# Performance work log

Hardware: AMD Instinct MI355X
Metric: run time of the kernel (lower is better)

Reference implementation:

```python
import jax, jax.numpy as jnp
import numpy as np

B, O, I = 128, 1024, 1024
EPS = 1e-07

def setup_inputs() -> dict:
    key = jax.random.key(0)
    ks = jax.random.split(key, 7)
    data = jax.random.normal(ks[0], (B, I), dtype=jnp.float32)
    # parameters, matching torch init: 2*rand-1, rand+0.1, 2*rand-1, ones+0.1, rand, rand
    input_x = 2.0 * jax.random.uniform(ks[1], (1, O, I), dtype=jnp.float32) - 1.0
    input_y = jax.random.uniform(ks[2], (1, O, I), dtype=jnp.float32) + 0.1
    output_x = 2.0 * jax.random.uniform(ks[3], (1, O, I), dtype=jnp.float32) - 1.0
    output_y = jnp.ones((1, O, I), dtype=jnp.float32) + 0.1
    linkage_add = jax.random.uniform(ks[4], (1, O, I), dtype=jnp.float32)
    linkage_mul = jax.random.uniform(ks[5], (1, O, I), dtype=jnp.float32)
    return {"data": data, "input_x": input_x, "input_y": input_y,
            "output_x": output_x, "output_y": output_y,
            "linkage_add": linkage_add, "linkage_mul": linkage_mul}

def reference(data, input_x, input_y, output_x, output_y, linkage_add, linkage_mul):
    shape = data.shape
    d = data.reshape(-1, 1, I)                      # (B,1,I)
    inp = input_x / input_y                          # (1,O,I)
    out = output_x / output_y                        # (1,O,I)
    tests = (inp + linkage_add) * (1.0 + linkage_mul)
    error = (tests - out) * jax.nn.sigmoid(d)        # (B,O,I)
    w = jax.nn.softmax(1.0 / jnp.sqrt(error * error + EPS), axis=1)
    expect = d * w                                   # (B,O,I)
    return jnp.sum(expect, axis=2).reshape(shape)
```

## Files before the change

### kernel.cpp

```cpp
#include <hip/hip_runtime.h>

#define B_ 128
#define O_ 1024
#define I_ 1024
#define NCHUNK 64
#define CI (I_ / NCHUNK)
#define WPB 4
#define TT_BYTES ((size_t)O_ * I_ * sizeof(float))

#define LOG2E_F  1.4426950408889634f
#define LN2_F    0.6931471805599453f
#define LN2SQ_F  0.4804530139182014f
#define EPSC_F   (1e-7f * LN2SQ_F)

typedef float v2f __attribute__((ext_vector_type(2)));

__device__ __forceinline__ float fast_rsq(float x)  { return __builtin_amdgcn_rsqf(x); }
__device__ __forceinline__ float fast_exp2(float x) { return __builtin_amdgcn_exp2f(x); }
__device__ __forceinline__ float fast_rcp(float x)  { return __builtin_amdgcn_rcpf(x); }

__device__ __forceinline__ float rfl(float x) {
    return __builtin_bit_cast(float,
        __builtin_amdgcn_readfirstlane(__builtin_bit_cast(int, x)));
}

template <int CTRL>
__device__ __forceinline__ float dpp_add(float v) {
    int x = __builtin_amdgcn_update_dpp(0, __builtin_bit_cast(int, v),
                                        CTRL, 0xf, 0xf, true);
    return v + __builtin_bit_cast(float, x);
}
__device__ __forceinline__ float wave_sum_uniform(float v) {
    v = dpp_add<0xB1>(v);
    v = dpp_add<0x4E>(v);
    v = dpp_add<0x141>(v);
    v = dpp_add<0x140>(v);
    v = dpp_add<0x142>(v);
    v = dpp_add<0x143>(v);
    return __builtin_bit_cast(float,
        __builtin_amdgcn_readlane(__builtin_bit_cast(int, v), 63));
}

__global__ __launch_bounds__(256) void build_T2_kernel(
    const float* __restrict__ ix, const float* __restrict__ iy,
    const float* __restrict__ ox, const float* __restrict__ oy,
    const float* __restrict__ la, const float* __restrict__ lm,
    float* __restrict__ Tt2, unsigned* __restrict__ minbits,
    float* __restrict__ out_zero)
{
    __shared__ float tile[32][33];
    __shared__ unsigned mloc[32];
    const int i0 = blockIdx.x * 32;
    const int o0 = blockIdx.y * 32;
    const int tx = threadIdx.x;
    const int ty = threadIdx.y;
    const int t  = ty * 32 + tx;

    if (t < 32) mloc[t] = 0xFFFFFFFFu;

    const int bid = blockIdx.y * gridDim.x + blockIdx.x;
    if (t < 128) out_zero[bid * 128 + t] = 0.0f;

#pragma unroll
    for (int r = 0; r < 32; r += 8) {
        const int o = o0 + ty + r;
        const int i = i0 + tx;
        const int idx = o * I_ + i;
        const float tt = fmaf(ix[idx] * fast_rcp(iy[idx]) + la[idx],
                              1.0f + lm[idx],
                              -(ox[idx] * fast_rcp(oy[idx])));
        tile[ty + r][tx] = tt * tt;
    }
    __syncthreads();
#pragma unroll
    for (int r = 0; r < 32; r += 8) {
        const int i = i0 + ty + r;
        const int o = o0 + tx;
        Tt2[i * O_ + o] = tile[tx][ty + r];
    }
    const int il = t & 31;
    const int g  = t >> 5;
    float mn = fminf(fminf(tile[4 * g + 0][il], tile[4 * g + 1][il]),
                     fminf(tile[4 * g + 2][il], tile[4 * g + 3][il]));
    atomicMin(&mloc[il], __builtin_bit_cast(unsigned, mn));
    __syncthreads();
    if (t < 32) atomicMin(&minbits[i0 + t], mloc[t]);
}

__global__ __launch_bounds__(256) void aeg_main_kernel(
    const float* __restrict__ data,
    const float* __restrict__ Tt2,
    const float* __restrict__ minr2,
    float* __restrict__ out)
{
    __shared__ float red[WPB][O_];

    const int w    = threadIdx.x >> 6;
    const int lane = threadIdx.x & 63;
    const int chunk = blockIdx.x * WPB + w;
    const int b     = blockIdx.y;

    const float4* rowbase = (const float4*)(Tt2 + (size_t)chunk * CI * O_);

    const float4* dv4 = (const float4*)(data + b * I_ + chunk * CI);
    const float4* mr4 = (const float4*)(minr2 + chunk * CI);
    float sdv[CI], ss2[CI], sm2[CI];
#pragma unroll
    for (int k = 0; k < 4; ++k) {
        const float4 a = dv4[k];
        const float4 m = mr4[k];
        const float av[4] = {a.x, a.y, a.z, a.w};
        const float mv[4] = {m.x, m.y, m.z, m.w};
#pragma unroll
        for (int j = 0; j < 4; ++j) {
            const float dv  = av[j];
            const float sig = fast_rcp(1.0f + fast_exp2(-dv * LOG2E_F));
            const float sc  = sig * LN2_F;
            const float s2  = sc * sc;
            const float m2  = fast_rsq(fmaf(mv[j], s2, EPSC_F));
            sdv[4 * k + j] = rfl(dv);
            ss2[4 * k + j] = rfl(s2);
            sm2[4 * k + j] = rfl(m2);
        }
    }

    v2f acc2[8];
#pragma unroll
    for (int j = 0; j < 8; ++j) acc2[j] = (v2f)0.0f;

    float4 rr[2][4];
#pragma unroll
    for (int k = 0; k < 4; ++k) rr[0][k] = rowbase[lane + 64 * k];

#pragma unroll
    for (int ii = 0; ii < CI; ++ii) {
        if (ii + 1 < CI) {
            const float4* nrow = rowbase + (size_t)(ii + 1) * (O_ / 4);
#pragma unroll
            for (int k = 0; k < 4; ++k) rr[(ii + 1) & 1][k] = nrow[lane + 64 * k];
        }
        float4* r = rr[ii & 1];
        const v2f s2v = {ss2[ii], ss2[ii]};
        const v2f m2v = {sm2[ii], sm2[ii]};
        const v2f epv = {EPSC_F, EPSC_F};

        v2f zv0 = (v2f)0.0f, zv1 = (v2f)0.0f;
#pragma unroll
        for (int k = 0; k < 4; ++k) {
            const v2f a = {r[k].x, r[k].y};
            const v2f c = {r[k].z, r[k].w};
            const v2f q0 = a * s2v + epv;
            const v2f q1 = c * s2v + epv;
            v2f t0, t1;
            t0.x = fast_rsq(q0.x); t0.y = fast_rsq(q0.y);
            t1.x = fast_rsq(q1.x); t1.y = fast_rsq(q1.y);
            t0 -= m2v;
            t1 -= m2v;
            r[k].x = fast_exp2(t0.x); r[k].y = fast_exp2(t0.y);
            r[k].z = fast_exp2(t1.x); r[k].w = fast_exp2(t1.y);
            zv0 += (v2f){r[k].x, r[k].y};
            zv1 += (v2f){r[k].z, r[k].w};
        }
        const v2f zv = zv0 + zv1;
        const float zt = wave_sum_uniform(zv.x + zv.y);
        const float scale = sdv[ii] * fast_rcp(zt);
        const v2f sc2 = {scale, scale};
#pragma unroll
        for (int k = 0; k < 4; ++k) {
            acc2[2 * k]     = (v2f){r[k].x, r[k].y} * sc2 + acc2[2 * k];
            acc2[2 * k + 1] = (v2f){r[k].z, r[k].w} * sc2 + acc2[2 * k + 1];
        }
    }

#pragma unroll
    for (int k = 0; k < 4; ++k) {
        float4 v;
        v.x = acc2[2 * k].x;     v.y = acc2[2 * k].y;
        v.z = acc2[2 * k + 1].x; v.w = acc2[2 * k + 1].y;
        ((float4*)&red[w][256 * k])[lane] = v;
    }
    __syncthreads();

    const int t = threadIdx.x;
    float4 v = ((const float4*)red[0])[t];
#pragma unroll
    for (int ww = 1; ww < WPB; ++ww) {
        const float4 u = ((const float4*)red[ww])[t];
        v.x += u.x; v.y += u.y; v.z += u.z; v.w += u.w;
    }
    float* ob = out + b * O_ + 4 * t;
    atomicAdd(&ob[0], v.x);
    atomicAdd(&ob[1], v.y);
    atomicAdd(&ob[2], v.z);
    atomicAdd(&ob[3], v.w);
}

extern "C" void kernel_launch(void* const* d_in, const int* in_sizes, int n_in,
                              void* d_out, int out_size, void* d_ws, size_t ws_size,
                              hipStream_t stream)
{
    const float* data = (const float*)d_in[0];
    const float* ix   = (const float*)d_in[1];
    const float* iy   = (const float*)d_in[2];
    const float* ox   = (const float*)d_in[3];
    const float* oy   = (const float*)d_in[4];
    const float* la   = (const float*)d_in[5];
    const float* lm   = (const float*)d_in[6];
    float* out  = (float*)d_out;
    float* Tt2  = (float*)d_ws;
    unsigned* minbits = (unsigned*)((char*)d_ws + TT_BYTES);

    (void)hipMemsetAsync(minbits, 0xFF, I_ * sizeof(unsigned), stream);

    build_T2_kernel<<<dim3(I_ / 32, O_ / 32), dim3(32, 8), 0, stream>>>(
        ix, iy, ox, oy, la, lm, Tt2, minbits, out);

    aeg_main_kernel<<<dim3(NCHUNK / WPB, B_), 256, 0, stream>>>(
        data, Tt2, (const float*)minbits, out);
}
```

Before: 122.0 us.

## Process two batch rows per wave to reuse each loaded T2 row

```diff
diff --git a/kernel.cpp b/kernel.cpp
--- a/kernel.cpp
+++ b/kernel.cpp
@@ -3,9 +3,10 @@
 #define B_ 128
 #define O_ 1024
 #define I_ 1024
-#define NCHUNK 64
+#define NCHUNK 128
 #define CI (I_ / NCHUNK)
 #define WPB 4
+#define BPW 2
 #define TT_BYTES ((size_t)O_ * I_ * sizeof(float))
 
 #define LOG2E_F  1.4426950408889634f
@@ -98,101 +99,164 @@
     const int w    = threadIdx.x >> 6;
     const int lane = threadIdx.x & 63;
     const int chunk = blockIdx.x * WPB + w;
-    const int b     = blockIdx.y;
+    const int b0    = blockIdx.y * BPW;
+    const int b1    = b0 + 1;
 
     const float4* rowbase = (const float4*)(Tt2 + (size_t)chunk * CI * O_);
 
-    const float4* dv4 = (const float4*)(data + b * I_ + chunk * CI);
+    const float4* d04 = (const float4*)(data + b0 * I_ + chunk * CI);
+    const float4* d14 = (const float4*)(data + b1 * I_ + chunk * CI);
     const float4* mr4 = (const float4*)(minr2 + chunk * CI);
-    float sdv[CI], ss2[CI], sm2[CI];
-#pragma unroll
-    for (int k = 0; k < 4; ++k) {
-        const float4 a = dv4[k];
-        const float4 m = mr4[k];
-        const float av[4] = {a.x, a.y, a.z, a.w};
-        const float mv[4] = {m.x, m.y, m.z, m.w};
+    float sdv0[CI], ss20[CI], sm20[CI];
+    float sdv1[CI], ss21[CI], sm21[CI];
+#pragma unroll
+    for (int k = 0; k < 2; ++k) {
+        const float4 a0 = d04[k];
+        const float4 a1 = d14[k];
+        const float4 m  = mr4[k];
+        const float a0v[4] = {a0.x, a0.y, a0.z, a0.w};
+        const float a1v[4] = {a1.x, a1.y, a1.z, a1.w};
+        const float mv[4]  = {m.x,  m.y,  m.z,  m.w};
 #pragma unroll
         for (int j = 0; j < 4; ++j) {
-            const float dv  = av[j];
-            const float sig = fast_rcp(1.0f + fast_exp2(-dv * LOG2E_F));
-            const float sc  = sig * LN2_F;
-            const float s2  = sc * sc;
-            const float m2  = fast_rsq(fmaf(mv[j], s2, EPSC_F));
-            sdv[4 * k + j] = rfl(dv);
-            ss2[4 * k + j] = rfl(s2);
-            sm2[4 * k + j] = rfl(m2);
-        }
-    }
-
-    v2f acc2[8];
-#pragma unroll
-    for (int j = 0; j < 8; ++j) acc2[j] = (v2f)0.0f;
-
-    float4 rr[2][4];
-#pragma unroll
-    for (int k = 0; k < 4; ++k) rr[0][k] = rowbase[lane + 64 * k];
+            const int idx = 4 * k + j;
+            {
+                const float dv  = a0v[j];
+                const float sig = fast_rcp(1.0f + fast_exp2(-dv * LOG2E_F));
+                const float sc  = sig * LN2_F;
+                const float s2  = sc * sc;
+                sdv0[idx] = rfl(dv);
+                ss20[idx] = rfl(s2);
+                sm20[idx] = rfl(fast_rsq(fmaf(mv[j], s2, EPSC_F)));
+            }
+            {
+                const float dv  = a1v[j];
+                const float sig = fast_rcp(1.0f + fast_exp2(-dv * LOG2E_F));
+                const float sc  = sig * LN2_F;
+                const float s2  = sc * sc;
+                sdv1[idx] = rfl(dv);
+                ss21[idx] = rfl(s2);
+                sm21[idx] = rfl(fast_rsq(fmaf(mv[j], s2, EPSC_F)));
+            }
+        }
+    }
+
+    v2f acc0[8], acc1[8];
+#pragma unroll
+    for (int j = 0; j < 8; ++j) { acc0[j] = (v2f)0.0f; acc1[j] = (v2f)0.0f; }
 
 #pragma unroll
     for (int ii = 0; ii < CI; ++ii) {
-        if (ii + 1 < CI) {
-            const float4* nrow = rowbase + (size_t)(ii + 1) * (O_ / 4);
-#pragma unroll
-            for (int k = 0; k < 4; ++k) rr[(ii + 1) & 1][k] = nrow[lane + 64 * k];
-        }
-        float4* r = rr[ii & 1];
-        const v2f s2v = {ss2[ii], ss2[ii]};
-        const v2f m2v = {sm2[ii], sm2[ii]};
-        const v2f epv = {EPSC_F, EPSC_F};
-
-        v2f zv0 = (v2f)0.0f, zv1 = (v2f)0.0f;
+        const float4* rowp = rowbase + (size_t)ii * (O_ / 4);
+        float4 r[4];
+#pragma unroll
+        for (int k = 0; k < 4; ++k) r[k] = rowp[lane + 64 * k];
+
+        const v2f s2v0 = {ss20[ii], ss20[ii]};
+        const v2f m2v0 = {sm20[ii], sm20[ii]};
+        const v2f epv  = {EPSC_F, EPSC_F};
+        float4 e0[4];
+        v2f z0a = (v2f)0.0f, z0b = (v2f)0.0f;
 #pragma unroll
         for (int k = 0; k < 4; ++k) {
             const v2f a = {r[k].x, r[k].y};
             const v2f c = {r[k].z, r[k].w};
-            const v2f q0 = a * s2v + epv;
-            const v2f q1 = c * s2v + epv;
+            const v2f q0 = a * s2v0 + epv;
+            const v2f q1 = c * s2v0 + epv;
             v2f t0, t1;
             t0.x = fast_rsq(q0.x); t0.y = fast_rsq(q0.y);
             t1.x = fast_rsq(q1.x); t1.y = fast_rsq(q1.y);
-            t0 -= m2v;
-            t1 -= m2v;
+            t0 -= m2v0;
+            t1 -= m2v0;
+            e0[k].x = fast_exp2(t0.x); e0[k].y = fast_exp2(t0.y);
+            e0[k].z = fast_exp2(t1.x); e0[k].w = fast_exp2(t1.y);
+            z0a += (v2f){e0[k].x, e0[k].y};
+            z0b += (v2f){e0[k].z, e0[k].w};
+        }
+        const v2f z0v = z0a + z0b;
+        const float zt0 = wave_sum_uniform(z0v.x + z0v.y);
+
+        const v2f s2v1 = {ss21[ii], ss21[ii]};
+        const v2f m2v1 = {sm21[ii], sm21[ii]};
+        v2f z1a = (v2f)0.0f, z1b = (v2f)0.0f;
+#pragma unroll
+        for (int k = 0; k < 4; ++k) {
+            const v2f a = {r[k].x, r[k].y};
+            const v2f c = {r[k].z, r[k].w};
+            const v2f q0 = a * s2v1 + epv;
+            const v2f q1 = c * s2v1 + epv;
+            v2f t0, t1;
+            t0.x = fast_rsq(q0.x); t0.y = fast_rsq(q0.y);
+            t1.x = fast_rsq(q1.x); t1.y = fast_rsq(q1.y);
+            t0 -= m2v1;
+            t1 -= m2v1;
             r[k].x = fast_exp2(t0.x); r[k].y = fast_exp2(t0.y);
             r[k].z = fast_exp2(t1.x); r[k].w = fast_exp2(t1.y);
-            zv0 += (v2f){r[k].x, r[k].y};
-            zv1 += (v2f){r[k].z, r[k].w};
-        }
-        const v2f zv = zv0 + zv1;
-        const float zt = wave_sum_uniform(zv.x + zv.y);
-        const float scale = sdv[ii] * fast_rcp(zt);
-        const v2f sc2 = {scale, scale};
-#pragma unroll
-        for (int k = 0; k < 4; ++k) {
-            acc2[2 * k]     = (v2f){r[k].x, r[k].y} * sc2 + acc2[2 * k];
-            acc2[2 * k + 1] = (v2f){r[k].z, r[k].w} * sc2 + acc2[2 * k + 1];
-        }
-    }
-
+            z1a += (v2f){r[k].x, r[k].y};
+            z1b += (v2f){r[k].z, r[k].w};
+        }
+        const float sc0 = sdv0[ii] * fast_rcp(zt0);
+        const v2f sc0v = {sc0, sc0};
+#pragma unroll
+        for (int k = 0; k < 4; ++k) {
+            acc0[2 * k]     = (v2f){e0[k].x, e0[k].y} * sc0v + acc0[2 * k];
+            acc0[2 * k + 1] = (v2f){e0[k].z, e0[k].w} * sc0v + acc0[2 * k + 1];
+        }
+        const v2f z1v = z1a + z1b;
+        const float zt1 = wave_sum_uniform(z1v.x + z1v.y);
+        const float sc1 = sdv1[ii] * fast_rcp(zt1);
+        const v2f sc1v = {sc1, sc1};
+#pragma unroll
+        for (int k = 0; k < 4; ++k) {
+            acc1[2 * k]     = (v2f){r[k].x, r[k].y} * sc1v + acc1[2 * k];
+            acc1[2 * k + 1] = (v2f){r[k].z, r[k].w} * sc1v + acc1[2 * k + 1];
+        }
+    }
+
+    const int t = threadIdx.x;
 #pragma unroll
     for (int k = 0; k < 4; ++k) {
         float4 v;
-        v.x = acc2[2 * k].x;     v.y = acc2[2 * k].y;
-        v.z = acc2[2 * k + 1].x; v.w = acc2[2 * k + 1].y;
+        v.x = acc0[2 * k].x;     v.y = acc0[2 * k].y;
+        v.z = acc0[2 * k + 1].x; v.w = acc0[2 * k + 1].y;
         ((float4*)&red[w][256 * k])[lane] = v;
     }
     __syncthreads();
-
-    const int t = threadIdx.x;
-    float4 v = ((const float4*)red[0])[t];
-#pragma unroll
-    for (int ww = 1; ww < WPB; ++ww) {
-        const float4 u = ((const float4*)red[ww])[t];
-        v.x += u.x; v.y += u.y; v.z += u.z; v.w += u.w;
-    }
-    float* ob = out + b * O_ + 4 * t;
-    atomicAdd(&ob[0], v.x);
-    atomicAdd(&ob[1], v.y);
-    atomicAdd(&ob[2], v.z);
-    atomicAdd(&ob[3], v.w);
+    {
+        float4 v = ((const float4*)red[0])[t];
+#pragma unroll
+        for (int ww = 1; ww < WPB; ++ww) {
+            const float4 u = ((const float4*)red[ww])[t];
+            v.x += u.x; v.y += u.y; v.z += u.z; v.w += u.w;
+        }
+        float* ob = out + b0 * O_ + 4 * t;
+        atomicAdd(&ob[0], v.x);
+        atomicAdd(&ob[1], v.y);
+        atomicAdd(&ob[2], v.z);
+        atomicAdd(&ob[3], v.w);
+    }
+    __syncthreads();
+#pragma unroll
+    for (int k = 0; k < 4; ++k) {
+        float4 v;
+        v.x = acc1[2 * k].x;     v.y = acc1[2 * k].y;
+        v.z = acc1[2 * k + 1].x; v.w = acc1[2 * k + 1].y;
+        ((float4*)&red[w][256 * k])[lane] = v;
+    }
+    __syncthreads();
+    {
+        float4 v = ((const float4*)red[0])[t];
+#pragma unroll
+        for (int ww = 1; ww < WPB; ++ww) {
+            const float4 u = ((const float4*)red[ww])[t];
+            v.x += u.x; v.y += u.y; v.z += u.z; v.w += u.w;
+        }
+        float* ob = out + b1 * O_ + 4 * t;
+        atomicAdd(&ob[0], v.x);
+        atomicAdd(&ob[1], v.y);
+        atomicAdd(&ob[2], v.z);
+        atomicAdd(&ob[3], v.w);
+    }
 }
 
 extern "C" void kernel_launch(void* const* d_in, const int* in_sizes, int n_in,
@@ -215,6 +279,6 @@
     build_T2_kernel<<<dim3(I_ / 32, O_ / 32), dim3(32, 8), 0, stream>>>(
         ix, iy, ox, oy, la, lm, Tt2, minbits, out);
 
-    aeg_main_kernel<<<dim3(NCHUNK / WPB, B_), 256, 0, stream>>>(
+    aeg_main_kernel<<<dim3(NCHUNK / WPB, B_ / BPW), 256, 0, stream>>>(
         data, Tt2, (const float*)minbits, out);
 }
```

New measurement: 148.4 us. 1.22x slower.
